# Kernel tuning notes

Hardware: AMD Instinct MI355X
Metric: run time of the kernel (lower is better)

## Reference

```python
import jax, jax.numpy as jnp
import numpy as np

D_MODEL = 1024
NUM_HEADS = 16
HEAD_DIM = D_MODEL // NUM_HEADS
DILATION = 2
SEGMENT = 1024
OFFSET = 0  # head_idx % dilation_rate; head_idx derived from a random param in torch, fixed to 0 here


def setup_inputs() -> dict:
    key = jax.random.key(0)
    x = jax.random.normal(key, (4, 8192, D_MODEL), dtype=jnp.float32)
    return {"x": x}


def reference(x):
    b, n, d = x.shape  # n is already a multiple of SEGMENT (no padding needed)
    n_seg = n // SEGMENT
    k = SEGMENT // DILATION  # sparse tokens kept per segment

    # dilated gather: within each segment keep every DILATION-th token
    local_idx = OFFSET + DILATION * jnp.arange(k)                      # [k]
    global_idx = SEGMENT * jnp.arange(n_seg)[:, None] + local_idx[None, :]  # [n_seg, k]
    xs = x[:, global_idx, :]                                           # [b, n_seg, k, d]

    # multi-head self-attention within each sparse segment (q = k = v = xs)
    qh = xs.reshape(b, n_seg, k, NUM_HEADS, HEAD_DIM)
    scale = 1.0 / jnp.sqrt(jnp.asarray(HEAD_DIM, dtype=xs.dtype))
    scores = jnp.einsum('bsqhd,bskhd->bshqk', qh, qh) * scale          # [b, n_seg, h, k, k]
    attn = jax.nn.softmax(scores, axis=-1)
    seg_out = jnp.einsum('bshqk,bskhd->bsqhd', attn, qh)
    a_os = seg_out.reshape(b, n_seg * k, d)                            # [b, M, d]

    # mix_outputs: denominator-weighted scatter-add merge back to full sequence
    idx = jnp.broadcast_to(global_idx.reshape(-1), (b, n_seg * k))     # [b, M] global positions
    a_denoms = a_os.sum(axis=-1)                                       # [b, M]

    def mix(o_b, den_b, idx_b):
        sums = jnp.zeros((n,), o_b.dtype).at[idx_b].add(den_b)         # scatter_add of denoms
        alphas = den_b / sums[idx_b]                                   # gather + divide
        return jnp.zeros((n, d), o_b.dtype).at[idx_b].add(o_b * alphas[:, None])

    return jax.vmap(mix)(a_os, a_denoms, idx)                          # [b, n, d]
```

## Files before the change

kernel.cpp:

```cpp
#include <hip/hip_runtime.h>
#include <math.h>

#define DM 1024
#define NSEQ 8192

typedef __attribute__((ext_vector_type(8))) short short8;
typedef __attribute__((ext_vector_type(4))) float floatx4;

__device__ __forceinline__ unsigned pk_rn(float a, float b) {
  return __builtin_amdgcn_perm(__float_as_uint(b) + 0x8000u,
                               __float_as_uint(a) + 0x8000u, 0x07060302u);
}

__device__ __forceinline__ void gload16(const uint4* g, uint4* l) {
  __builtin_amdgcn_global_load_lds((const __attribute__((address_space(1))) void*)g,
                                   (__attribute__((address_space(3))) void*)l, 16, 0, 0);
}

__global__ __launch_bounds__(256, 4)
void prep_kernel(const float* __restrict__ x, uint4* __restrict__ kbf,
                 uint4* __restrict__ vt, float* __restrict__ out) {
  __shared__ uint4 T[1024];
  const int bid = blockIdx.x;
  const int tau = bid >> 2, c = bid & 3;
  const int b = tau >> 7, s = (tau >> 4) & 7, h = tau & 15;
  const float* xb = x + ((size_t)b * NSEQ + s * 1024) * DM + h * 64;
  float* ob = out + ((size_t)b * NSEQ + s * 1024) * DM + h * 64;
  const int tid = threadIdx.x;
  const int c8 = tid & 7, rr = tid >> 3;

  const float4 z = make_float4(0.f, 0.f, 0.f, 0.f);
  #pragma unroll
  for (int p = 0; p < 4; ++p) {
    int r = p * 32 + rr;
    int g = c * 128 + r;
    const float* src = xb + (size_t)(2 * g) * DM + c8 * 8;
    float4 A = *(const float4*)src;
    float4 B = *(const float4*)(src + 4);
    uint4 pk;
    pk.x = pk_rn(A.x, A.y); pk.y = pk_rn(A.z, A.w);
    pk.z = pk_rn(B.x, B.y); pk.w = pk_rn(B.z, B.w);
    T[r * 8 + (c8 ^ (r & 7))] = pk;
    float* zp = ob + (size_t)(2 * g + 1) * DM + c8 * 8;
    *(float4*)zp = z;
    *(float4*)(zp + 4) = z;
  }
  __syncthreads();

  uint4* kdst = kbf + (size_t)tau * 4096 + c * 1024;
  #pragma unroll
  for (int p = 0; p < 4; ++p) {
    int L = p * 256 + tid;
    kdst[L] = T[L];
  }
  const unsigned short* Ts = (const unsigned short*)T;
  uint4* vdst = vt + (size_t)tau * 4096 + c * 1024;
  #pragma unroll
  for (int p = 0; p < 4; ++p) {
    int M = p * 256 + tid;
    int u16 = M >> 6, dp = M & 63;
    int d = dp ^ (u16 & 7);
    unsigned v[8];
    #pragma unroll
    for (int j = 0; j < 8; ++j) {
      int kk = 8 * u16 + j;
      v[j] = Ts[(kk * 8 + ((d >> 3) ^ (kk & 7))) * 8 + (d & 7)];
    }
    uint4 pk;
    pk.x = v[0] | (v[1] << 16);
    pk.y = v[2] | (v[3] << 16);
    pk.z = v[4] | (v[5] << 16);
    pk.w = v[6] | (v[7] << 16);
    vdst[M] = pk;
  }
}

__global__ __launch_bounds__(512, 4)
void attn_kernel(const uint4* __restrict__ kbf, const uint4* __restrict__ vt,
                 float* __restrict__ out) {
  __shared__ uint4 smem[3072];
  const int bid = blockIdx.x;
  const int bs = (bid & 7) | ((bid >> 8) << 3);
  const int inner = (bid >> 3) & 31;
  const int h = inner >> 1, qh = inner & 1;
  const int b = bs >> 3, s = bs & 7;
  const int tau = bs * 16 + h;
  const uint4* KT = kbf + (size_t)tau * 4096;
  const uint4* VTg = vt + (size_t)tau * 4096;
  float* ob = out + ((size_t)b * NSEQ + s * 1024) * DM + h * 64;
  const int tid = threadIdx.x;
  const int lane = tid & 63;
  const int wu = __builtin_amdgcn_readfirstlane(tid >> 6);
  const int cq = lane & 15, u = lane >> 4;
  const int qw0 = qh * 256 + wu * 32;

  short8 qf[2][2];
  #pragma unroll
  for (int qs = 0; qs < 2; ++qs) {
    int R = qw0 + qs * 16 + cq;
    #pragma unroll
    for (int ksd = 0; ksd < 2; ++ksd)
      qf[qs][ksd] = *(const short8*)&KT[(size_t)R * 8 + ((4 * ksd + u) ^ (cq & 7))];
  }

  floatx4 o[2][4];
  #pragma unroll
  for (int qs = 0; qs < 2; ++qs)
    #pragma unroll
    for (int nt = 0; nt < 4; ++nt) o[qs][nt] = (floatx4){0.f, 0.f, 0.f, 0.f};
  float l[2] = {0.f, 0.f};
  const float cf = 0.125f * 1.44269504088896340736f;

  unsigned short* Pw = (unsigned short*)&smem[2048 + wu * 128];
  const int pswz = u ^ (cq & 3);

  for (int c = 0; c < 4; ++c) {
    {
      const uint4* kg = KT + c * 1024 + wu * 128 + lane;
      const uint4* vg = VTg + c * 1024 + wu * 128 + lane;
      gload16(kg, &smem[wu * 128]);
      gload16(kg + 64, &smem[wu * 128 + 64]);
      gload16(vg, &smem[1024 + wu * 128]);
      gload16(vg + 64, &smem[1024 + wu * 128 + 64]);
    }
    __syncthreads();

    #pragma unroll
    for (int ks = 0; ks < 4; ++ks) {
      floatx4 acc[2][2];
      #pragma unroll
      for (int qs = 0; qs < 2; ++qs)
        #pragma unroll
        for (int t = 0; t < 2; ++t) acc[qs][t] = (floatx4){0.f, 0.f, 0.f, 0.f};
      #pragma unroll
      for (int t = 0; t < 2; ++t) {
        int r = 16 * (2 * ks + t) + cq;
        #pragma unroll
        for (int ksd = 0; ksd < 2; ++ksd) {
          short8 af = *(short8*)&smem[r * 8 + ((4 * ksd + u) ^ (cq & 7))];
          #pragma unroll
          for (int qs = 0; qs < 2; ++qs)
            acc[qs][t] = __builtin_amdgcn_mfma_f32_16x16x32_bf16(af, qf[qs][ksd], acc[qs][t], 0, 0, 0);
        }
      }
      #pragma unroll
      for (int qs = 0; qs < 2; ++qs)
        #pragma unroll
        for (int t = 0; t < 2; ++t) {
          float p0 = __builtin_amdgcn_exp2f(acc[qs][t][0] * cf);
          float p1 = __builtin_amdgcn_exp2f(acc[qs][t][1] * cf);
          float p2 = __builtin_amdgcn_exp2f(acc[qs][t][2] * cf);
          float p3 = __builtin_amdgcn_exp2f(acc[qs][t][3] * cf);
          l[qs] += (p0 + p1) + (p2 + p3);
          uint2 w2;
          w2.x = pk_rn(p0, p1);
          w2.y = pk_rn(p2, p3);
          int unit = (qs * 16 + cq) * 4 + ((2 * t + (u >> 1)) ^ (cq & 3));
          *(uint2*)(Pw + unit * 8 + (u & 1) * 4) = w2;
        }
      const int u16 = 4 * ks + u;
      short8 vfr[4];
      #pragma unroll
      for (int nt = 0; nt < 4; ++nt)
        vfr[nt] = *(short8*)&smem[1024 + u16 * 64 + 16 * nt + (cq ^ (u16 & 7))];
      #pragma unroll
      for (int qs = 0; qs < 2; ++qs) {
        short8 pf = *(short8*)(Pw + ((qs * 16 + cq) * 4 + pswz) * 8);
        #pragma unroll
        for (int nt = 0; nt < 4; ++nt)
          o[qs][nt] = __builtin_amdgcn_mfma_f32_16x16x32_bf16(pf, vfr[nt], o[qs][nt], 0, 0, 0);
      }
    }
    __syncthreads();
  }

  #pragma unroll
  for (int qs = 0; qs < 2; ++qs) {
    float lf = l[qs];
    lf += __shfl_xor(lf, 16, 64);
    lf += __shfl_xor(lf, 32, 64);
    #pragma unroll
    for (int r = 0; r < 4; ++r) {
      float linv = 1.f / __shfl(lf, 4 * u + r, 64);
      float* orow = ob + (size_t)(2 * (qw0 + qs * 16 + 4 * u + r)) * DM + cq;
      #pragma unroll
      for (int nt = 0; nt < 4; ++nt)
        orow[nt * 16] = o[qs][nt][r] * linv;
    }
  }
}

#define CH 128
#define KTS 72
#define VTS 136
#define PS  136

__device__ __forceinline__ unsigned pk_bf16x2(float a, float b) {
  unsigned x = __float_as_uint(a), y = __float_as_uint(b);
  x += 0x7fffu + ((x >> 16) & 1u);
  y += 0x7fffu + ((y >> 16) & 1u);
  return (x >> 16) | (y & 0xffff0000u);
}

__global__ __launch_bounds__(256, 4)
void dilattn_fallback(const float* __restrict__ x, float* __restrict__ out) {
  __shared__ unsigned short Kt[CH * KTS];
  __shared__ unsigned short VT[64 * VTS];
  const int i = blockIdx.x;
  const int bs = (i & 7) | ((i >> 10) << 3);
  const int hq = (i >> 3) & 127;
  const int b = bs >> 3, s = bs & 7;
  const int h = hq >> 3, qt = hq & 7;
  const float* xb = x + ((size_t)b * NSEQ + (size_t)s * 1024) * DM;
  float* outb = out + ((size_t)b * NSEQ + (size_t)s * 1024) * DM;
  const int tid = threadIdx.x;
  const int lane = tid & 63;
  const int w = tid >> 6;
  const int cq = lane & 15;
  const int u = lane >> 4;
  const int q0 = qt * 64 + w * 16;
  {
    const float4 z = make_float4(0.f, 0.f, 0.f, 0.f);
    #pragma unroll
    for (int it = 0; it < 4; ++it) {
      int idx = tid + 256 * it;
      int j = idx >> 4, c4 = idx & 15;
      *(float4*)(outb + (size_t)(2 * (qt * 64 + j) + 1) * DM + h * 64 + c4 * 4) = z;
    }
  }
  short8 qf[2];
  {
    const float* xq = xb + (size_t)(2 * (q0 + cq)) * DM + h * 64;
    #pragma unroll
    for (int ks = 0; ks < 2; ++ks) {
      float4 a = *(const float4*)(xq + 32 * ks + 8 * u);
      float4 c = *(const float4*)(xq + 32 * ks + 8 * u + 4);
      union { unsigned u4[4]; short8 s8; } pk;
      pk.u4[0] = pk_bf16x2(a.x, a.y);
      pk.u4[1] = pk_bf16x2(a.z, a.w);
      pk.u4[2] = pk_bf16x2(c.x, c.y);
      pk.u4[3] = pk_bf16x2(c.z, c.w);
      qf[ks] = pk.s8;
    }
  }
  floatx4 o[4];
  #pragma unroll
  for (int nt = 0; nt < 4; ++nt) o[nt] = (floatx4){0.f, 0.f, 0.f, 0.f};
  float l = 0.f;
  const float cf = 0.125f * 1.44269504088896340736f;
  const int c8 = tid & 7;
  const int sr = tid >> 3;
  const int vd = tid & 63;
  const int vg = tid >> 6;
  for (int c = 0; c < 4; ++c) {
    #pragma unroll
    for (int pass = 0; pass < 4; ++pass) {
      int r = pass * 32 + sr;
      const float* src = xb + (size_t)(2 * (c * CH + r)) * DM + h * 64 + c8 * 8;
      float4 a = *(const float4*)(src);
      float4 d2 = *(const float4*)(src + 4);
      union { unsigned u4[4]; short8 s8; } pk;
      pk.u4[0] = pk_bf16x2(a.x, a.y);
      pk.u4[1] = pk_bf16x2(a.z, a.w);
      pk.u4[2] = pk_bf16x2(d2.x, d2.y);
      pk.u4[3] = pk_bf16x2(d2.z, d2.w);
      *(short8*)(Kt + r * KTS + c8 * 8) = pk.s8;
    }
    #pragma unroll
    for (int g8 = 0; g8 < 4; ++g8) {
      float v[8];
      #pragma unroll
      for (int j = 0; j < 8; ++j)
        v[j] = xb[(size_t)(2 * (c * CH + vg * 32 + g8 * 8 + j)) * DM + h * 64 + vd];
      union { unsigned u4[4]; short8 s8; } pk;
      #pragma unroll
      for (int m = 0; m < 4; ++m) pk.u4[m] = pk_bf16x2(v[2 * m], v[2 * m + 1]);
      *(short8*)(VT + vd * VTS + vg * 32 + g8 * 8) = pk.s8;
    }
    __syncthreads();
    floatx4 st[8];
    #pragma unroll
    for (int t = 0; t < 8; ++t) {
      floatx4 acc = {0.f, 0.f, 0.f, 0.f};
      #pragma unroll
      for (int ks = 0; ks < 2; ++ks) {
        short8 af = *(short8*)(Kt + (t * 16 + cq) * KTS + 32 * ks + 8 * u);
        acc = __builtin_amdgcn_mfma_f32_16x16x32_bf16(af, qf[ks], acc, 0, 0, 0);
      }
      st[t] = acc;
    }
    #pragma unroll
    for (int t = 0; t < 8; ++t)
      #pragma unroll
      for (int r = 0; r < 4; ++r) {
        float p = __builtin_amdgcn_exp2f(st[t][r] * cf);
        st[t][r] = p;
        l += p;
      }
    __syncthreads();
    unsigned short* Pw = Kt + w * 16 * PS;
    #pragma unroll
    for (int t = 0; t < 8; ++t) {
      uint2 pk2;
      pk2.x = pk_bf16x2(st[t][0], st[t][1]);
      pk2.y = pk_bf16x2(st[t][2], st[t][3]);
      *(uint2*)(Pw + cq * PS + t * 16 + 4 * u) = pk2;
    }
    #pragma unroll
    for (int ks = 0; ks < 4; ++ks) {
      short8 pf = *(short8*)(Pw + cq * PS + 32 * ks + 8 * u);
      #pragma unroll
      for (int nt = 0; nt < 4; ++nt) {
        short8 vf = *(short8*)(VT + (nt * 16 + cq) * VTS + 32 * ks + 8 * u);
        o[nt] = __builtin_amdgcn_mfma_f32_16x16x32_bf16(pf, vf, o[nt], 0, 0, 0);
      }
    }
    __syncthreads();
  }
  l += __shfl_xor(l, 16, 64);
  l += __shfl_xor(l, 32, 64);
  float linv[4];
  #pragma unroll
  for (int r = 0; r < 4; ++r) linv[r] = 1.f / __shfl(l, 4 * u + r, 64);
  #pragma unroll
  for (int r = 0; r < 4; ++r) {
    float* orow = outb + (size_t)(2 * (q0 + 4 * u + r)) * DM + h * 64 + cq;
    #pragma unroll
    for (int nt = 0; nt < 4; ++nt)
      orow[nt * 16] = o[nt][r] * linv[r];
  }
}

extern "C" void kernel_launch(void* const* d_in, const int* in_sizes, int n_in,
                              void* d_out, int out_size, void* d_ws, size_t ws_size,
                              hipStream_t stream) {
  const float* x = (const float*)d_in[0];
  float* out = (float*)d_out;
  if (ws_size >= (size_t)67108864) {
    uint4* kbf = (uint4*)d_ws;
    uint4* vt = kbf + (size_t)512 * 4096;
    prep_kernel<<<dim3(2048), dim3(256), 0, stream>>>(x, kbf, vt, out);
    attn_kernel<<<dim3(1024), dim3(512), 0, stream>>>(kbf, vt, out);
  } else {
    dilattn_fallback<<<dim3(4096), dim3(256), 0, stream>>>(x, out);
  }
}
```

Measured before the change: 266.0 us.

## Fuse bf16 prep and attention into one kernel with LDS-resident K and V^T

Replaces the prep kernel plus attention kernel with a single fused kernel. Each block now handles a whole (batch, segment, head) tile. It loads all 512 sparse tokens into LDS as bf16 and builds each V^T chunk in LDS, double-buffered, while computing on the previous chunk. This removes the workspace round-trip of K and V^T through global memory and one kernel launch. The cost is a smaller grid (512 blocks) with 64 queries per wave, so register pressure and LDS use (112KB) rise and occupancy falls.

```diff
diff --git a/kernel.cpp b/kernel.cpp
--- a/kernel.cpp
+++ b/kernel.cpp
@@ -1,5 +1,4 @@
 #include <hip/hip_runtime.h>
-#include <math.h>
 
 #define DM 1024
 #define NSEQ 8192
@@ -12,170 +11,157 @@
                                __float_as_uint(a) + 0x8000u, 0x07060302u);
 }
 
-__device__ __forceinline__ void gload16(const uint4* g, uint4* l) {
-  __builtin_amdgcn_global_load_lds((const __attribute__((address_space(1))) void*)g,
-                                   (__attribute__((address_space(3))) void*)l, 16, 0, 0);
-}
 
-__global__ __launch_bounds__(256, 4)
-void prep_kernel(const float* __restrict__ x, uint4* __restrict__ kbf,
-                 uint4* __restrict__ vt, float* __restrict__ out) {
-  __shared__ uint4 T[1024];
-  const int bid = blockIdx.x;
-  const int tau = bid >> 2, c = bid & 3;
-  const int b = tau >> 7, s = (tau >> 4) & 7, h = tau & 15;
-  const float* xb = x + ((size_t)b * NSEQ + s * 1024) * DM + h * 64;
-  float* ob = out + ((size_t)b * NSEQ + s * 1024) * DM + h * 64;
-  const int tid = threadIdx.x;
-  const int c8 = tid & 7, rr = tid >> 3;
-
-  const float4 z = make_float4(0.f, 0.f, 0.f, 0.f);
+__device__ __forceinline__ void build_vt(uint4* smem, int tid, int c, int buf) {
+  const unsigned short* Ts = (const unsigned short*)smem;
+  uint4* vb = &smem[4096 + buf * 1024];
   #pragma unroll
-  for (int p = 0; p < 4; ++p) {
-    int r = p * 32 + rr;
-    int g = c * 128 + r;
-    const float* src = xb + (size_t)(2 * g) * DM + c8 * 8;
-    float4 A = *(const float4*)src;
-    float4 B = *(const float4*)(src + 4);
-    uint4 pk;
-    pk.x = pk_rn(A.x, A.y); pk.y = pk_rn(A.z, A.w);
-    pk.z = pk_rn(B.x, B.y); pk.w = pk_rn(B.z, B.w);
-    T[r * 8 + (c8 ^ (r & 7))] = pk;
-    float* zp = ob + (size_t)(2 * g + 1) * DM + c8 * 8;
-    *(float4*)zp = z;
-    *(float4*)(zp + 4) = z;
-  }
-  __syncthreads();
-
-  uint4* kdst = kbf + (size_t)tau * 4096 + c * 1024;
-  #pragma unroll
-  for (int p = 0; p < 4; ++p) {
-    int L = p * 256 + tid;
-    kdst[L] = T[L];
-  }
-  const unsigned short* Ts = (const unsigned short*)T;
-  uint4* vdst = vt + (size_t)tau * 4096 + c * 1024;
-  #pragma unroll
-  for (int p = 0; p < 4; ++p) {
-    int M = p * 256 + tid;
-    int u16 = M >> 6, dp = M & 63;
+  for (int p = 0; p < 2; ++p) {
+    int m = p * 512 + tid;
+    int u16 = m >> 6, dp = m & 63;
     int d = dp ^ (u16 & 7);
     unsigned v[8];
     #pragma unroll
     for (int j = 0; j < 8; ++j) {
-      int kk = 8 * u16 + j;
-      v[j] = Ts[(kk * 8 + ((d >> 3) ^ (kk & 7))) * 8 + (d & 7)];
+      int kk = c * 128 + 8 * u16 + j;
+      v[j] = Ts[(kk * 8 + ((d >> 3) ^ j)) * 8 + (d & 7)];
     }
     uint4 pk;
     pk.x = v[0] | (v[1] << 16);
     pk.y = v[2] | (v[3] << 16);
     pk.z = v[4] | (v[5] << 16);
     pk.w = v[6] | (v[7] << 16);
-    vdst[M] = pk;
+    vb[m] = pk;
   }
 }
 
-__global__ __launch_bounds__(512, 4)
-void attn_kernel(const uint4* __restrict__ kbf, const uint4* __restrict__ vt,
-                 float* __restrict__ out) {
-  __shared__ uint4 smem[3072];
-  const int bid = blockIdx.x;
-  const int bs = (bid & 7) | ((bid >> 8) << 3);
-  const int inner = (bid >> 3) & 31;
-  const int h = inner >> 1, qh = inner & 1;
-  const int b = bs >> 3, s = bs & 7;
-  const int tau = bs * 16 + h;
-  const uint4* KT = kbf + (size_t)tau * 4096;
-  const uint4* VTg = vt + (size_t)tau * 4096;
+__global__ __launch_bounds__(512, 2)
+void fused_kernel(const float* __restrict__ x, float* __restrict__ out) {
+  __shared__ uint4 smem[7168];
+  const int tau = blockIdx.x;
+  const int b = tau >> 7, s = (tau >> 4) & 7, h = tau & 15;
+  const float* xb = x + ((size_t)b * NSEQ + s * 1024) * DM + h * 64;
   float* ob = out + ((size_t)b * NSEQ + s * 1024) * DM + h * 64;
   const int tid = threadIdx.x;
   const int lane = tid & 63;
   const int wu = __builtin_amdgcn_readfirstlane(tid >> 6);
+
+  {
+    const int c8 = tid & 7, rr = tid >> 3;
+    float4 A[8], B[8];
+    #pragma unroll
+    for (int p = 0; p < 8; ++p) {
+      int r = p * 64 + rr;
+      const float* src = xb + (size_t)(2 * r) * DM + c8 * 8;
+      A[p] = *(const float4*)src;
+      B[p] = *(const float4*)(src + 4);
+    }
+    const float4 z = make_float4(0.f, 0.f, 0.f, 0.f);
+    #pragma unroll
+    for (int p = 0; p < 8; ++p) {
+      int r = p * 64 + rr;
+      float* zp = ob + (size_t)(2 * r + 1) * DM + c8 * 8;
+      *(float4*)zp = z;
+      *(float4*)(zp + 4) = z;
+    }
+    #pragma unroll
+    for (int p = 0; p < 8; ++p) {
+      int r = p * 64 + rr;
+      uint4 pk;
+      pk.x = pk_rn(A[p].x, A[p].y); pk.y = pk_rn(A[p].z, A[p].w);
+      pk.z = pk_rn(B[p].x, B[p].y); pk.w = pk_rn(B[p].z, B[p].w);
+      smem[r * 8 + (c8 ^ (r & 7))] = pk;
+    }
+  }
+  __syncthreads();
+
   const int cq = lane & 15, u = lane >> 4;
-  const int qw0 = qh * 256 + wu * 32;
+  const int qw0 = wu * 64;
 
-  short8 qf[2][2];
+  short8 qf[4][2];
   #pragma unroll
-  for (int qs = 0; qs < 2; ++qs) {
+  for (int qs = 0; qs < 4; ++qs) {
     int R = qw0 + qs * 16 + cq;
     #pragma unroll
     for (int ksd = 0; ksd < 2; ++ksd)
-      qf[qs][ksd] = *(const short8*)&KT[(size_t)R * 8 + ((4 * ksd + u) ^ (cq & 7))];
+      qf[qs][ksd] = *(const short8*)&smem[R * 8 + ((4 * ksd + u) ^ (cq & 7))];
   }
 
-  floatx4 o[2][4];
+  build_vt(smem, tid, 0, 0);
+  __syncthreads();
+
+  floatx4 o[4][4];
   #pragma unroll
-  for (int qs = 0; qs < 2; ++qs)
+  for (int qs = 0; qs < 4; ++qs)
     #pragma unroll
     for (int nt = 0; nt < 4; ++nt) o[qs][nt] = (floatx4){0.f, 0.f, 0.f, 0.f};
-  float l[2] = {0.f, 0.f};
+  float l[4] = {0.f, 0.f, 0.f, 0.f};
   const float cf = 0.125f * 1.44269504088896340736f;
 
-  unsigned short* Pw = (unsigned short*)&smem[2048 + wu * 128];
+  unsigned short* Pw = (unsigned short*)&smem[6144 + wu * 128];
   const int pswz = u ^ (cq & 3);
 
   for (int c = 0; c < 4; ++c) {
-    {
-      const uint4* kg = KT + c * 1024 + wu * 128 + lane;
-      const uint4* vg = VTg + c * 1024 + wu * 128 + lane;
-      gload16(kg, &smem[wu * 128]);
-      gload16(kg + 64, &smem[wu * 128 + 64]);
-      gload16(vg, &smem[1024 + wu * 128]);
-      gload16(vg + 64, &smem[1024 + wu * 128 + 64]);
-    }
-    __syncthreads();
+    if (c < 3) build_vt(smem, tid, c + 1, (c + 1) & 1);
+    const uint4* vbase = &smem[4096 + (c & 1) * 1024];
 
     #pragma unroll
     for (int ks = 0; ks < 4; ++ks) {
-      floatx4 acc[2][2];
+      floatx4 acc[4][2];
       #pragma unroll
-      for (int qs = 0; qs < 2; ++qs)
+      for (int qs = 0; qs < 4; ++qs)
         #pragma unroll
         for (int t = 0; t < 2; ++t) acc[qs][t] = (floatx4){0.f, 0.f, 0.f, 0.f};
       #pragma unroll
       for (int t = 0; t < 2; ++t) {
-        int r = 16 * (2 * ks + t) + cq;
+        int R = c * 128 + 32 * ks + 16 * t + cq;
         #pragma unroll
         for (int ksd = 0; ksd < 2; ++ksd) {
-          short8 af = *(short8*)&smem[r * 8 + ((4 * ksd + u) ^ (cq & 7))];
+          short8 af = *(short8*)&smem[R * 8 + ((4 * ksd + u) ^ (cq & 7))];
           #pragma unroll
-          for (int qs = 0; qs < 2; ++qs)
+          for (int qs = 0; qs < 4; ++qs)
             acc[qs][t] = __builtin_amdgcn_mfma_f32_16x16x32_bf16(af, qf[qs][ksd], acc[qs][t], 0, 0, 0);
         }
       }
-      #pragma unroll
-      for (int qs = 0; qs < 2; ++qs)
-        #pragma unroll
-        for (int t = 0; t < 2; ++t) {
-          float p0 = __builtin_amdgcn_exp2f(acc[qs][t][0] * cf);
-          float p1 = __builtin_amdgcn_exp2f(acc[qs][t][1] * cf);
-          float p2 = __builtin_amdgcn_exp2f(acc[qs][t][2] * cf);
-          float p3 = __builtin_amdgcn_exp2f(acc[qs][t][3] * cf);
-          l[qs] += (p0 + p1) + (p2 + p3);
-          uint2 w2;
-          w2.x = pk_rn(p0, p1);
-          w2.y = pk_rn(p2, p3);
-          int unit = (qs * 16 + cq) * 4 + ((2 * t + (u >> 1)) ^ (cq & 3));
-          *(uint2*)(Pw + unit * 8 + (u & 1) * 4) = w2;
-        }
       const int u16 = 4 * ks + u;
       short8 vfr[4];
       #pragma unroll
       for (int nt = 0; nt < 4; ++nt)
-        vfr[nt] = *(short8*)&smem[1024 + u16 * 64 + 16 * nt + (cq ^ (u16 & 7))];
+        vfr[nt] = *(const short8*)&vbase[u16 * 64 + 16 * nt + (cq ^ (u16 & 7))];
       #pragma unroll
-      for (int qs = 0; qs < 2; ++qs) {
-        short8 pf = *(short8*)(Pw + ((qs * 16 + cq) * 4 + pswz) * 8);
+      for (int qp = 0; qp < 2; ++qp) {
         #pragma unroll
-        for (int nt = 0; nt < 4; ++nt)
-          o[qs][nt] = __builtin_amdgcn_mfma_f32_16x16x32_bf16(pf, vfr[nt], o[qs][nt], 0, 0, 0);
+        for (int q2 = 0; q2 < 2; ++q2) {
+          int qs = 2 * qp + q2;
+          #pragma unroll
+          for (int t = 0; t < 2; ++t) {
+            float p0 = __builtin_amdgcn_exp2f(acc[qs][t][0] * cf);
+            float p1 = __builtin_amdgcn_exp2f(acc[qs][t][1] * cf);
+            float p2 = __builtin_amdgcn_exp2f(acc[qs][t][2] * cf);
+            float p3 = __builtin_amdgcn_exp2f(acc[qs][t][3] * cf);
+            l[qs] += (p0 + p1) + (p2 + p3);
+            uint2 w2;
+            w2.x = pk_rn(p0, p1);
+            w2.y = pk_rn(p2, p3);
+            int unit = (q2 * 16 + cq) * 4 + ((2 * t + (u >> 1)) ^ (cq & 3));
+            *(uint2*)(Pw + unit * 8 + (u & 1) * 4) = w2;
+          }
+        }
+        #pragma unroll
+        for (int q2 = 0; q2 < 2; ++q2) {
+          int qs = 2 * qp + q2;
+          short8 pf = *(short8*)(Pw + ((q2 * 16 + cq) * 4 + pswz) * 8);
+          #pragma unroll
+          for (int nt = 0; nt < 4; ++nt)
+            o[qs][nt] = __builtin_amdgcn_mfma_f32_16x16x32_bf16(pf, vfr[nt], o[qs][nt], 0, 0, 0);
+        }
       }
     }
-    __syncthreads();
+    if (c < 3) __syncthreads();
   }
 
   #pragma unroll
-  for (int qs = 0; qs < 2; ++qs) {
+  for (int qs = 0; qs < 4; ++qs) {
     float lf = l[qs];
     lf += __shfl_xor(lf, 16, 64);
     lf += __shfl_xor(lf, 32, 64);
@@ -190,158 +176,10 @@
   }
 }
 
-#define CH 128
-#define KTS 72
-#define VTS 136
-#define PS  136
-
-__device__ __forceinline__ unsigned pk_bf16x2(float a, float b) {
-  unsigned x = __float_as_uint(a), y = __float_as_uint(b);
-  x += 0x7fffu + ((x >> 16) & 1u);
-  y += 0x7fffu + ((y >> 16) & 1u);
-  return (x >> 16) | (y & 0xffff0000u);
-}
-
-__global__ __launch_bounds__(256, 4)
-void dilattn_fallback(const float* __restrict__ x, float* __restrict__ out) {
-  __shared__ unsigned short Kt[CH * KTS];
-  __shared__ unsigned short VT[64 * VTS];
-  const int i = blockIdx.x;
-  const int bs = (i & 7) | ((i >> 10) << 3);
-  const int hq = (i >> 3) & 127;
-  const int b = bs >> 3, s = bs & 7;
-  const int h = hq >> 3, qt = hq & 7;
-  const float* xb = x + ((size_t)b * NSEQ + (size_t)s * 1024) * DM;
-  float* outb = out + ((size_t)b * NSEQ + (size_t)s * 1024) * DM;
-  const int tid = threadIdx.x;
-  const int lane = tid & 63;
-  const int w = tid >> 6;
-  const int cq = lane & 15;
-  const int u = lane >> 4;
-  const int q0 = qt * 64 + w * 16;
-  {
-    const float4 z = make_float4(0.f, 0.f, 0.f, 0.f);
-    #pragma unroll
-    for (int it = 0; it < 4; ++it) {
-      int idx = tid + 256 * it;
-      int j = idx >> 4, c4 = idx & 15;
-      *(float4*)(outb + (size_t)(2 * (qt * 64 + j) + 1) * DM + h * 64 + c4 * 4) = z;
-    }
-  }
-  short8 qf[2];
-  {
-    const float* xq = xb + (size_t)(2 * (q0 + cq)) * DM + h * 64;
-    #pragma unroll
-    for (int ks = 0; ks < 2; ++ks) {
-      float4 a = *(const float4*)(xq + 32 * ks + 8 * u);
-      float4 c = *(const float4*)(xq + 32 * ks + 8 * u + 4);
-      union { unsigned u4[4]; short8 s8; } pk;
-      pk.u4[0] = pk_bf16x2(a.x, a.y);
-      pk.u4[1] = pk_bf16x2(a.z, a.w);
-      pk.u4[2] = pk_bf16x2(c.x, c.y);
-      pk.u4[3] = pk_bf16x2(c.z, c.w);
-      qf[ks] = pk.s8;
-    }
-  }
-  floatx4 o[4];
-  #pragma unroll
-  for (int nt = 0; nt < 4; ++nt) o[nt] = (floatx4){0.f, 0.f, 0.f, 0.f};
-  float l = 0.f;
-  const float cf = 0.125f * 1.44269504088896340736f;
-  const int c8 = tid & 7;
-  const int sr = tid >> 3;
-  const int vd = tid & 63;
-  const int vg = tid >> 6;
-  for (int c = 0; c < 4; ++c) {
-    #pragma unroll
-    for (int pass = 0; pass < 4; ++pass) {
-      int r = pass * 32 + sr;
-      const float* src = xb + (size_t)(2 * (c * CH + r)) * DM + h * 64 + c8 * 8;
-      float4 a = *(const float4*)(src);
-      float4 d2 = *(const float4*)(src + 4);
-      union { unsigned u4[4]; short8 s8; } pk;
-      pk.u4[0] = pk_bf16x2(a.x, a.y);
-      pk.u4[1] = pk_bf16x2(a.z, a.w);
-      pk.u4[2] = pk_bf16x2(d2.x, d2.y);
-      pk.u4[3] = pk_bf16x2(d2.z, d2.w);
-      *(short8*)(Kt + r * KTS + c8 * 8) = pk.s8;
-    }
-    #pragma unroll
-    for (int g8 = 0; g8 < 4; ++g8) {
-      float v[8];
-      #pragma unroll
-      for (int j = 0; j < 8; ++j)
-        v[j] = xb[(size_t)(2 * (c * CH + vg * 32 + g8 * 8 + j)) * DM + h * 64 + vd];
-      union { unsigned u4[4]; short8 s8; } pk;
-      #pragma unroll
-      for (int m = 0; m < 4; ++m) pk.u4[m] = pk_bf16x2(v[2 * m], v[2 * m + 1]);
-      *(short8*)(VT + vd * VTS + vg * 32 + g8 * 8) = pk.s8;
-    }
-    __syncthreads();
-    floatx4 st[8];
-    #pragma unroll
-    for (int t = 0; t < 8; ++t) {
-      floatx4 acc = {0.f, 0.f, 0.f, 0.f};
-      #pragma unroll
-      for (int ks = 0; ks < 2; ++ks) {
-        short8 af = *(short8*)(Kt + (t * 16 + cq) * KTS + 32 * ks + 8 * u);
-        acc = __builtin_amdgcn_mfma_f32_16x16x32_bf16(af, qf[ks], acc, 0, 0, 0);
-      }
-      st[t] = acc;
-    }
-    #pragma unroll
-    for (int t = 0; t < 8; ++t)
-      #pragma unroll
-      for (int r = 0; r < 4; ++r) {
-        float p = __builtin_amdgcn_exp2f(st[t][r] * cf);
-        st[t][r] = p;
-        l += p;
-      }
-    __syncthreads();
-    unsigned short* Pw = Kt + w * 16 * PS;
-    #pragma unroll
-    for (int t = 0; t < 8; ++t) {
-      uint2 pk2;
-      pk2.x = pk_bf16x2(st[t][0], st[t][1]);
-      pk2.y = pk_bf16x2(st[t][2], st[t][3]);
-      *(uint2*)(Pw + cq * PS + t * 16 + 4 * u) = pk2;
-    }
-    #pragma unroll
-    for (int ks = 0; ks < 4; ++ks) {
-      short8 pf = *(short8*)(Pw + cq * PS + 32 * ks + 8 * u);
-      #pragma unroll
-      for (int nt = 0; nt < 4; ++nt) {
-        short8 vf = *(short8*)(VT + (nt * 16 + cq) * VTS + 32 * ks + 8 * u);
-        o[nt] = __builtin_amdgcn_mfma_f32_16x16x32_bf16(pf, vf, o[nt], 0, 0, 0);
-      }
-    }
-    __syncthreads();
-  }
-  l += __shfl_xor(l, 16, 64);
-  l += __shfl_xor(l, 32, 64);
-  float linv[4];
-  #pragma unroll
-  for (int r = 0; r < 4; ++r) linv[r] = 1.f / __shfl(l, 4 * u + r, 64);
-  #pragma unroll
-  for (int r = 0; r < 4; ++r) {
-    float* orow = outb + (size_t)(2 * (q0 + 4 * u + r)) * DM + h * 64 + cq;
-    #pragma unroll
-    for (int nt = 0; nt < 4; ++nt)
-      orow[nt * 16] = o[nt][r] * linv[r];
-  }
-}
-
 extern "C" void kernel_launch(void* const* d_in, const int* in_sizes, int n_in,
                               void* d_out, int out_size, void* d_ws, size_t ws_size,
                               hipStream_t stream) {
   const float* x = (const float*)d_in[0];
   float* out = (float*)d_out;
-  if (ws_size >= (size_t)67108864) {
-    uint4* kbf = (uint4*)d_ws;
-    uint4* vt = kbf + (size_t)512 * 4096;
-    prep_kernel<<<dim3(2048), dim3(256), 0, stream>>>(x, kbf, vt, out);
-    attn_kernel<<<dim3(1024), dim3(512), 0, stream>>>(kbf, vt, out);
-  } else {
-    dilattn_fallback<<<dim3(4096), dim3(256), 0, stream>>>(x, out);
-  }
+  fused_kernel<<<dim3(512), dim3(512), 0, stream>>>(x, out);
 }
```

New measurement: 293.5 us. 1.1x slower.
